# Kernel tuning notes

Hardware: AMD Instinct MI355X
Metric: run time of the kernel (lower is better)

## Reference

```python
import jax, jax.numpy as jnp
import numpy as np

ITERATIONS = 20


def setup_inputs() -> dict:
    key = jax.random.key(0)
    x = jax.random.normal(key, (64, 8, 256, 256), dtype=jnp.float32)
    return {"x": x}


def reference(x):
    # Sinkhorn operator in log space: 20 alternating row/col log-softmax,
    # then exponentiate to obtain a (soft) doubly-stochastic matrix.
    def body(i, x):
        x = jax.nn.log_softmax(x, axis=-2)  # normalize columns
        x = jax.nn.log_softmax(x, axis=-1)  # normalize rows
        return x

    x = jax.lax.fori_loop(0, ITERATIONS, body, x)
    return jnp.exp(x)
```

## Files before the change

kernel.cpp:

```cpp
#include <hip/hip_runtime.h>

#define MAT_N 256
#define TPB   512
#define ITERS 20

typedef _Float16 half2v __attribute__((ext_vector_type(2)));

template<int CTRL>
__device__ __forceinline__ float dpp_add(float x) {
    int s = __builtin_amdgcn_update_dpp(0, __builtin_bit_cast(int, x), CTRL, 0xF, 0xF, true);
    return x + __builtin_bit_cast(float, s);
}
__device__ __forceinline__ float allreduce16(float x) {
    x = dpp_add<0x121>(x);
    x = dpp_add<0x122>(x);
    x = dpp_add<0x124>(x);
    x = dpp_add<0x128>(x);
    return x;
}

__device__ __forceinline__ half2v pkrtz(float lo, float hi) {
    return __builtin_bit_cast(half2v, __builtin_amdgcn_cvt_pkrtz(lo, hi));
}

#if __has_builtin(__builtin_amdgcn_fdot2)
__device__ __forceinline__ float dot2(half2v a, half2v b, float c) {
    return __builtin_amdgcn_fdot2(a, b, c, false);
}
#else
__device__ __forceinline__ float dot2(half2v a, half2v b, float c) {
    return c + (float)a.x * (float)b.x + (float)a.y * (float)b.y;
}
#endif

__global__ __launch_bounds__(TPB)
__attribute__((amdgpu_waves_per_eu(4, 4)))
void sinkhorn_kernel(const float* __restrict__ x, float* __restrict__ out)
{
    const int t    = threadIdx.x;
    const int tC   = t & 15;
    const int tR   = t >> 4;
    const int row0 = tR << 3;
    const int col0 = tC << 4;

    const size_t moff = (size_t)blockIdx.x * (MAT_N * MAT_N);
    const float* __restrict__ xm = x + moff;
    float* __restrict__       om = out + moff;

    __shared__ half2v part[32][132];
    __shared__ float  gvec[MAT_N];

    half2v E[8][8];
#pragma unroll
    for (int l = 0; l < 8; ++l) {
        const float* rp = xm + (row0 + l) * MAT_N + col0;
        float4 a = ((const float4*)rp)[0];
        float4 b = ((const float4*)rp)[1];
        float4 c = ((const float4*)rp)[2];
        float4 d = ((const float4*)rp)[3];
        E[l][0] = (half2v){(_Float16)__expf(a.x), (_Float16)__expf(a.y)};
        E[l][1] = (half2v){(_Float16)__expf(a.z), (_Float16)__expf(a.w)};
        E[l][2] = (half2v){(_Float16)__expf(b.x), (_Float16)__expf(b.y)};
        E[l][3] = (half2v){(_Float16)__expf(b.z), (_Float16)__expf(b.w)};
        E[l][4] = (half2v){(_Float16)__expf(c.x), (_Float16)__expf(c.y)};
        E[l][5] = (half2v){(_Float16)__expf(c.z), (_Float16)__expf(c.w)};
        E[l][6] = (half2v){(_Float16)__expf(d.x), (_Float16)__expf(d.y)};
        E[l][7] = (half2v){(_Float16)__expf(d.z), (_Float16)__expf(d.w)};
    }

    float  f[8];
    half2v f2[8];
#pragma unroll
    for (int l = 0; l < 8; ++l) {
        f[l]  = 1.0f;
        f2[l] = (half2v){(_Float16)1.0f, (_Float16)1.0f};
    }
    half2v g2[8];

    for (int it = 0; it < ITERS; ++it) {
        half2v p2[8];
#pragma unroll
        for (int k = 0; k < 8; ++k) p2[k] = E[0][k] * f2[0];
#pragma unroll
        for (int l = 1; l < 8; ++l)
#pragma unroll
            for (int k = 0; k < 8; ++k) p2[k] += E[l][k] * f2[l];

        {
            half2v* wp = &part[tR][tC << 3];
            float4 w0 = make_float4(__builtin_bit_cast(float, p2[0]),
                                    __builtin_bit_cast(float, p2[1]),
                                    __builtin_bit_cast(float, p2[2]),
                                    __builtin_bit_cast(float, p2[3]));
            float4 w1 = make_float4(__builtin_bit_cast(float, p2[4]),
                                    __builtin_bit_cast(float, p2[5]),
                                    __builtin_bit_cast(float, p2[6]),
                                    __builtin_bit_cast(float, p2[7]));
            ((float4*)wp)[0] = w0;
            ((float4*)wp)[1] = w1;
        }
        __syncthreads();

        if (t < 128) {
            float slo = 0.0f, shi = 0.0f;
#pragma unroll
            for (int r = 0; r < 32; ++r) {
                half2v v = part[r][t];
                slo += (float)v.x;
                shi += (float)v.y;
            }
            float2 gw;
            gw.x = __builtin_amdgcn_rcpf(slo);
            gw.y = __builtin_amdgcn_rcpf(shi);
            *(float2*)&gvec[t << 1] = gw;
        }
        __syncthreads();

        {
            const float* gp = &gvec[col0];
            float4 a = ((const float4*)gp)[0];
            float4 b = ((const float4*)gp)[1];
            float4 c = ((const float4*)gp)[2];
            float4 d = ((const float4*)gp)[3];
            g2[0] = pkrtz(a.x, a.y);
            g2[1] = pkrtz(a.z, a.w);
            g2[2] = pkrtz(b.x, b.y);
            g2[3] = pkrtz(b.z, b.w);
            g2[4] = pkrtz(c.x, c.y);
            g2[5] = pkrtz(c.z, c.w);
            g2[6] = pkrtz(d.x, d.y);
            g2[7] = pkrtz(d.z, d.w);
        }

#pragma unroll
        for (int l = 0; l < 8; ++l) {
            float s = dot2(E[l][0], g2[0], 0.0f);
#pragma unroll
            for (int k = 1; k < 8; ++k) s = dot2(E[l][k], g2[k], s);
            s = allreduce16(s);
            f[l] = __builtin_amdgcn_rcpf(s);
            _Float16 h = (_Float16)f[l];
            f2[l] = (half2v){h, h};
        }
    }

    float g[16];
    {
        const float* gp = &gvec[col0];
        float4 a = ((const float4*)gp)[0];
        float4 b = ((const float4*)gp)[1];
        float4 c = ((const float4*)gp)[2];
        float4 d = ((const float4*)gp)[3];
        g[0]=a.x;  g[1]=a.y;  g[2]=a.z;  g[3]=a.w;
        g[4]=b.x;  g[5]=b.y;  g[6]=b.z;  g[7]=b.w;
        g[8]=c.x;  g[9]=c.y;  g[10]=c.z; g[11]=c.w;
        g[12]=d.x; g[13]=d.y; g[14]=d.z; g[15]=d.w;
    }
#pragma unroll
    for (int l = 0; l < 8; ++l) {
        float fr = f[l];
        float* rp = om + (row0 + l) * MAT_N + col0;
        float o[16];
#pragma unroll
        for (int k = 0; k < 8; ++k) {
            o[2*k]   = (float)E[l][k].x * fr * g[2*k];
            o[2*k+1] = (float)E[l][k].y * fr * g[2*k+1];
        }
        ((float4*)rp)[0] = make_float4(o[0],  o[1],  o[2],  o[3]);
        ((float4*)rp)[1] = make_float4(o[4],  o[5],  o[6],  o[7]);
        ((float4*)rp)[2] = make_float4(o[8],  o[9],  o[10], o[11]);
        ((float4*)rp)[3] = make_float4(o[12], o[13], o[14], o[15]);
    }
}

extern "C" void kernel_launch(void* const* d_in, const int* in_sizes, int n_in,
                              void* d_out, int out_size, void* d_ws, size_t ws_size,
                              hipStream_t stream) {
    const float* x = (const float*)d_in[0];
    float* out = (float*)d_out;
    const int nmat = in_sizes[0] / (MAT_N * MAT_N);
    sinkhorn_kernel<<<nmat, TPB, 0, stream>>>(x, out);
}
```

Baseline: 270.8 us.

## Parallelize column-sum reduction across all threads with DPP and padded LDS

The column reduction is spread over all 512 threads instead of only 128. Each thread sums 8 of the 32 partial rows, and the four partial sums are combined with DPP row shifts. The partial buffer is padded to a new stride with per-group offsets to avoid LDS bank conflicts. The reciprocal g is also stored pre-packed as fp16 pairs, so the broadcast read becomes two 16-byte loads with no conversion. This shortens the serial reduction phase between barriers, at the cost of more complex indexing and extra LDS.

```diff
diff --git a/kernel.cpp b/kernel.cpp
--- a/kernel.cpp
+++ b/kernel.cpp
@@ -3,6 +3,7 @@
 #define MAT_N 256
 #define TPB   512
 #define ITERS 20
+#define PSTRIDE 164
 
 typedef _Float16 half2v __attribute__((ext_vector_type(2)));
 
@@ -18,6 +19,11 @@
     x = dpp_add<0x128>(x);
     return x;
 }
+__device__ __forceinline__ float reduce4spaced(float x) {
+    x = dpp_add<0x124>(x);
+    x = dpp_add<0x128>(x);
+    return x;
+}
 
 __device__ __forceinline__ half2v pkrtz(float lo, float hi) {
     return __builtin_bit_cast(half2v, __builtin_amdgcn_cvt_pkrtz(lo, hi));
@@ -32,6 +38,7 @@
     return c + (float)a.x * (float)b.x + (float)a.y * (float)b.y;
 }
 #endif
+
 
 __global__ __launch_bounds__(TPB)
 __attribute__((amdgpu_waves_per_eu(4, 4)))
@@ -42,12 +49,19 @@
     const int tR   = t >> 4;
     const int row0 = tR << 3;
     const int col0 = tC << 4;
+    const int pbase = (tC << 3) + ((tC >> 2) << 2);
+
+    const int rl   = t & 15;
+    const int rw   = ((t >> 4) << 2) + (rl & 3);
+    const int rrow = rl >> 2;
+    const int rpos = rw + ((rw >> 5) << 2);
 
     const size_t moff = (size_t)blockIdx.x * (MAT_N * MAT_N);
     const float* __restrict__ xm = x + moff;
     float* __restrict__       om = out + moff;
 
-    __shared__ half2v part[32][132];
+    __shared__ half2v part[32 * PSTRIDE];
+    __shared__ half2v g2p[140];
     __shared__ float  gvec[MAT_N];
 
     half2v E[8][8];
@@ -77,6 +91,9 @@
     }
     half2v g2[8];
 
+    half2v* const wp = &part[tR * PSTRIDE + pbase];
+    const half2v* const rdp = &part[rrow * PSTRIDE + rpos];
+
     for (int it = 0; it < ITERS; ++it) {
         half2v p2[8];
 #pragma unroll
@@ -87,7 +104,6 @@
             for (int k = 0; k < 8; ++k) p2[k] += E[l][k] * f2[l];
 
         {
-            half2v* wp = &part[tR][tC << 3];
             float4 w0 = make_float4(__builtin_bit_cast(float, p2[0]),
                                     __builtin_bit_cast(float, p2[1]),
                                     __builtin_bit_cast(float, p2[2]),
@@ -97,39 +113,40 @@
                                     __builtin_bit_cast(float, p2[6]),
                                     __builtin_bit_cast(float, p2[7]));
             ((float4*)wp)[0] = w0;
-            ((float4*)wp)[1] = w1;
+            ((float4*)(wp + 4))[0] = w1;
         }
         __syncthreads();
 
-        if (t < 128) {
+        {
             float slo = 0.0f, shi = 0.0f;
 #pragma unroll
-            for (int r = 0; r < 32; ++r) {
-                half2v v = part[r][t];
+            for (int i = 0; i < 8; ++i) {
+                half2v v = rdp[(i << 2) * PSTRIDE];
                 slo += (float)v.x;
                 shi += (float)v.y;
             }
-            float2 gw;
-            gw.x = __builtin_amdgcn_rcpf(slo);
-            gw.y = __builtin_amdgcn_rcpf(shi);
-            *(float2*)&gvec[t << 1] = gw;
+            slo = reduce4spaced(slo);
+            shi = reduce4spaced(shi);
+            if (rl < 4) {
+                float glo = __builtin_amdgcn_rcpf(slo);
+                float ghi = __builtin_amdgcn_rcpf(shi);
+                *(float2*)&gvec[rw << 1] = make_float2(glo, ghi);
+                g2p[rpos] = pkrtz(glo, ghi);
+            }
         }
         __syncthreads();
 
         {
-            const float* gp = &gvec[col0];
-            float4 a = ((const float4*)gp)[0];
-            float4 b = ((const float4*)gp)[1];
-            float4 c = ((const float4*)gp)[2];
-            float4 d = ((const float4*)gp)[3];
-            g2[0] = pkrtz(a.x, a.y);
-            g2[1] = pkrtz(a.z, a.w);
-            g2[2] = pkrtz(b.x, b.y);
-            g2[3] = pkrtz(b.z, b.w);
-            g2[4] = pkrtz(c.x, c.y);
-            g2[5] = pkrtz(c.z, c.w);
-            g2[6] = pkrtz(d.x, d.y);
-            g2[7] = pkrtz(d.z, d.w);
+            const float4 ga = ((const float4*)&g2p[pbase])[0];
+            const float4 gb = ((const float4*)&g2p[pbase + 4])[0];
+            g2[0] = __builtin_bit_cast(half2v, ga.x);
+            g2[1] = __builtin_bit_cast(half2v, ga.y);
+            g2[2] = __builtin_bit_cast(half2v, ga.z);
+            g2[3] = __builtin_bit_cast(half2v, ga.w);
+            g2[4] = __builtin_bit_cast(half2v, gb.x);
+            g2[5] = __builtin_bit_cast(half2v, gb.y);
+            g2[6] = __builtin_bit_cast(half2v, gb.z);
+            g2[7] = __builtin_bit_cast(half2v, gb.w);
         }
 
 #pragma unroll
```

After: 259.4 us. 1.04x faster.

## Keep transposed copy of E in registers for DPP-based column reductions

Applied to the files above, without the earlier changes.

Builds a transposed fp16 copy of the exp matrix in registers through a shared-memory staging pass. Column sums then use the same dot2-plus-DPP reduction pattern as row sums. This replaces the shared-memory partial-sum write and the serial 32-row reduction done by 128 threads. Each iteration now exchanges only the f and g scaling vectors through small padded LDS buffers. The cost is doubled register storage for E (high pressure at 4 waves/EU) and a one-time transpose with extra barriers.

```diff
diff --git a/kernel.cpp b/kernel.cpp
--- a/kernel.cpp
+++ b/kernel.cpp
@@ -3,6 +3,7 @@
 #define MAT_N 256
 #define TPB   512
 #define ITERS 20
+#define TSTRIDE 72
 
 typedef _Float16 half2v __attribute__((ext_vector_type(2)));
 
@@ -18,11 +19,9 @@
     x = dpp_add<0x128>(x);
     return x;
 }
-
 __device__ __forceinline__ half2v pkrtz(float lo, float hi) {
     return __builtin_bit_cast(half2v, __builtin_amdgcn_cvt_pkrtz(lo, hi));
 }
-
 #if __has_builtin(__builtin_amdgcn_fdot2)
 __device__ __forceinline__ float dot2(half2v a, half2v b, float c) {
     return __builtin_amdgcn_fdot2(a, b, c, false);
@@ -38,17 +37,23 @@
 void sinkhorn_kernel(const float* __restrict__ x, float* __restrict__ out)
 {
     const int t    = threadIdx.x;
-    const int tC   = t & 15;
-    const int tR   = t >> 4;
-    const int row0 = tR << 3;
-    const int col0 = tC << 4;
+    const int g16  = t >> 4;
+    const int rl   = t & 15;
+    const int row0 = g16 << 3;
+    const int col0 = rl << 4;
+
+    const int pb_fg  = (rl << 3) + ((rl >> 2) << 2);
+    const int wWrite = (g16 << 2) + rl;
+    const int pWrite = wWrite + ((wWrite >> 5) << 2);
 
     const size_t moff = (size_t)blockIdx.x * (MAT_N * MAT_N);
     const float* __restrict__ xm = x + moff;
     float* __restrict__       om = out + moff;
 
-    __shared__ half2v part[32][132];
-    __shared__ float  gvec[MAT_N];
+    __shared__ __align__(16) _Float16 stage[256 * TSTRIDE];
+    __shared__ __align__(16) half2v   fbuf[140];
+    __shared__ __align__(16) half2v   gbuf[140];
+    __shared__ float2 gf[128];
 
     half2v E[8][8];
 #pragma unroll
@@ -68,103 +73,122 @@
         E[l][7] = (half2v){(_Float16)__expf(d.z), (_Float16)__expf(d.w)};
     }
 
-    float  f[8];
-    half2v f2[8];
+    if (t < 140) fbuf[t] = (half2v){(_Float16)1.0f, (_Float16)1.0f};
+
+    half2v ET[8][8];
+#pragma unroll
+    for (int q = 0; q < 4; ++q) {
+        if ((rl >> 2) == q) {
+            const int coff = (rl & 3) << 4;
+#pragma unroll
+            for (int l = 0; l < 8; ++l) {
+                const int idx = (row0 + l) * TSTRIDE + coff;
+                *(float4*)&stage[idx] = make_float4(
+                    __builtin_bit_cast(float, E[l][0]), __builtin_bit_cast(float, E[l][1]),
+                    __builtin_bit_cast(float, E[l][2]), __builtin_bit_cast(float, E[l][3]));
+                *(float4*)&stage[idx + 8] = make_float4(
+                    __builtin_bit_cast(float, E[l][4]), __builtin_bit_cast(float, E[l][5]),
+                    __builtin_bit_cast(float, E[l][6]), __builtin_bit_cast(float, E[l][7]));
+            }
+        }
+        __syncthreads();
+        if ((g16 >> 3) == q) {
+            const int coff = (g16 & 7) << 3;
+#pragma unroll
+            for (int j = 0; j < 8; ++j) {
+                float4 ra = *(const float4*)&stage[((rl << 4) + (j << 1)) * TSTRIDE + coff];
+                float4 rb = *(const float4*)&stage[((rl << 4) + (j << 1) + 1) * TSTRIDE + coff];
+                half2v a0 = __builtin_bit_cast(half2v, ra.x), b0 = __builtin_bit_cast(half2v, rb.x);
+                half2v a1 = __builtin_bit_cast(half2v, ra.y), b1 = __builtin_bit_cast(half2v, rb.y);
+                half2v a2 = __builtin_bit_cast(half2v, ra.z), b2 = __builtin_bit_cast(half2v, rb.z);
+                half2v a3 = __builtin_bit_cast(half2v, ra.w), b3 = __builtin_bit_cast(half2v, rb.w);
+                ET[0][j] = (half2v){a0.x, b0.x};  ET[1][j] = (half2v){a0.y, b0.y};
+                ET[2][j] = (half2v){a1.x, b1.x};  ET[3][j] = (half2v){a1.y, b1.y};
+                ET[4][j] = (half2v){a2.x, b2.x};  ET[5][j] = (half2v){a2.y, b2.y};
+                ET[6][j] = (half2v){a3.x, b3.x};  ET[7][j] = (half2v){a3.y, b3.y};
+            }
+        }
+        __syncthreads();
+    }
+
+    float fv[8];
+
+    for (int it = 0; it < ITERS; ++it) {
+        float4 fa = *(const float4*)&fbuf[pb_fg];
+        float4 fb = *(const float4*)&fbuf[pb_fg + 4];
+        half2v fp0 = __builtin_bit_cast(half2v, fa.x), fp1 = __builtin_bit_cast(half2v, fa.y);
+        half2v fp2 = __builtin_bit_cast(half2v, fa.z), fp3 = __builtin_bit_cast(half2v, fa.w);
+        half2v fp4 = __builtin_bit_cast(half2v, fb.x), fp5 = __builtin_bit_cast(half2v, fb.y);
+        half2v fp6 = __builtin_bit_cast(half2v, fb.z), fp7 = __builtin_bit_cast(half2v, fb.w);
+
+        float gv[8];
+#pragma unroll
+        for (int c = 0; c < 8; ++c) {
+            float s = dot2(ET[c][0], fp0, 0.0f);
+            s = dot2(ET[c][1], fp1, s);
+            s = dot2(ET[c][2], fp2, s);
+            s = dot2(ET[c][3], fp3, s);
+            s = dot2(ET[c][4], fp4, s);
+            s = dot2(ET[c][5], fp5, s);
+            s = dot2(ET[c][6], fp6, s);
+            s = dot2(ET[c][7], fp7, s);
+            s = allreduce16(s);
+            gv[c] = __builtin_amdgcn_rcpf(s);
+        }
+        {
+            float glo = rl == 1 ? gv[2] : rl == 2 ? gv[4] : rl == 3 ? gv[6] : gv[0];
+            float ghi = rl == 1 ? gv[3] : rl == 2 ? gv[5] : rl == 3 ? gv[7] : gv[1];
+            if (rl < 4) {
+                gbuf[pWrite] = pkrtz(glo, ghi);
+                if (it == ITERS - 1) gf[wWrite] = make_float2(glo, ghi);
+            }
+        }
+        __syncthreads();
+
+        float4 ga = *(const float4*)&gbuf[pb_fg];
+        float4 gb = *(const float4*)&gbuf[pb_fg + 4];
+        half2v g0 = __builtin_bit_cast(half2v, ga.x), g1 = __builtin_bit_cast(half2v, ga.y);
+        half2v g2 = __builtin_bit_cast(half2v, ga.z), g3 = __builtin_bit_cast(half2v, ga.w);
+        half2v g4 = __builtin_bit_cast(half2v, gb.x), g5 = __builtin_bit_cast(half2v, gb.y);
+        half2v g6 = __builtin_bit_cast(half2v, gb.z), g7 = __builtin_bit_cast(half2v, gb.w);
+
+#pragma unroll
+        for (int l = 0; l < 8; ++l) {
+            float s = dot2(E[l][0], g0, 0.0f);
+            s = dot2(E[l][1], g1, s);
+            s = dot2(E[l][2], g2, s);
+            s = dot2(E[l][3], g3, s);
+            s = dot2(E[l][4], g4, s);
+            s = dot2(E[l][5], g5, s);
+            s = dot2(E[l][6], g6, s);
+            s = dot2(E[l][7], g7, s);
+            s = allreduce16(s);
+            fv[l] = __builtin_amdgcn_rcpf(s);
+        }
+        {
+            float flo = rl == 1 ? fv[2] : rl == 2 ? fv[4] : rl == 3 ? fv[6] : fv[0];
+            float fhi = rl == 1 ? fv[3] : rl == 2 ? fv[5] : rl == 3 ? fv[7] : fv[1];
+            if (rl < 4) fbuf[pWrite] = pkrtz(flo, fhi);
+        }
+        __syncthreads();
+    }
+
+    float Gc[16];
+#pragma unroll
+    for (int i = 0; i < 8; ++i) {
+        float2 gg = gf[(rl << 3) + i];
+        Gc[2 * i]     = gg.x;
+        Gc[2 * i + 1] = gg.y;
+    }
 #pragma unroll
     for (int l = 0; l < 8; ++l) {
-        f[l]  = 1.0f;
-        f2[l] = (half2v){(_Float16)1.0f, (_Float16)1.0f};
-    }
-    half2v g2[8];
-
-    for (int it = 0; it < ITERS; ++it) {
-        half2v p2[8];
-#pragma unroll
-        for (int k = 0; k < 8; ++k) p2[k] = E[0][k] * f2[0];
-#pragma unroll
-        for (int l = 1; l < 8; ++l)
-#pragma unroll
-            for (int k = 0; k < 8; ++k) p2[k] += E[l][k] * f2[l];
-
-        {
-            half2v* wp = &part[tR][tC << 3];
-            float4 w0 = make_float4(__builtin_bit_cast(float, p2[0]),
-                                    __builtin_bit_cast(float, p2[1]),
-                                    __builtin_bit_cast(float, p2[2]),
-                                    __builtin_bit_cast(float, p2[3]));
-            float4 w1 = make_float4(__builtin_bit_cast(float, p2[4]),
-                                    __builtin_bit_cast(float, p2[5]),
-                                    __builtin_bit_cast(float, p2[6]),
-                                    __builtin_bit_cast(float, p2[7]));
-            ((float4*)wp)[0] = w0;
-            ((float4*)wp)[1] = w1;
-        }
-        __syncthreads();
-
-        if (t < 128) {
-            float slo = 0.0f, shi = 0.0f;
-#pragma unroll
-            for (int r = 0; r < 32; ++r) {
-                half2v v = part[r][t];
-                slo += (float)v.x;
-                shi += (float)v.y;
-            }
-            float2 gw;
-            gw.x = __builtin_amdgcn_rcpf(slo);
-            gw.y = __builtin_amdgcn_rcpf(shi);
-            *(float2*)&gvec[t << 1] = gw;
-        }
-        __syncthreads();
-
-        {
-            const float* gp = &gvec[col0];
-            float4 a = ((const float4*)gp)[0];
-            float4 b = ((const float4*)gp)[1];
-            float4 c = ((const float4*)gp)[2];
-            float4 d = ((const float4*)gp)[3];
-            g2[0] = pkrtz(a.x, a.y);
-            g2[1] = pkrtz(a.z, a.w);
-            g2[2] = pkrtz(b.x, b.y);
-            g2[3] = pkrtz(b.z, b.w);
-            g2[4] = pkrtz(c.x, c.y);
-            g2[5] = pkrtz(c.z, c.w);
-            g2[6] = pkrtz(d.x, d.y);
-            g2[7] = pkrtz(d.z, d.w);
-        }
-
-#pragma unroll
-        for (int l = 0; l < 8; ++l) {
-            float s = dot2(E[l][0], g2[0], 0.0f);
-#pragma unroll
-            for (int k = 1; k < 8; ++k) s = dot2(E[l][k], g2[k], s);
-            s = allreduce16(s);
-            f[l] = __builtin_amdgcn_rcpf(s);
-            _Float16 h = (_Float16)f[l];
-            f2[l] = (half2v){h, h};
-        }
-    }
-
-    float g[16];
-    {
-        const float* gp = &gvec[col0];
-        float4 a = ((const float4*)gp)[0];
-        float4 b = ((const float4*)gp)[1];
-        float4 c = ((const float4*)gp)[2];
-        float4 d = ((const float4*)gp)[3];
-        g[0]=a.x;  g[1]=a.y;  g[2]=a.z;  g[3]=a.w;
-        g[4]=b.x;  g[5]=b.y;  g[6]=b.z;  g[7]=b.w;
-        g[8]=c.x;  g[9]=c.y;  g[10]=c.z; g[11]=c.w;
-        g[12]=d.x; g[13]=d.y; g[14]=d.z; g[15]=d.w;
-    }
-#pragma unroll
-    for (int l = 0; l < 8; ++l) {
-        float fr = f[l];
+        float fr = fv[l];
         float* rp = om + (row0 + l) * MAT_N + col0;
         float o[16];
 #pragma unroll
         for (int k = 0; k < 8; ++k) {
-            o[2*k]   = (float)E[l][k].x * fr * g[2*k];
-            o[2*k+1] = (float)E[l][k].y * fr * g[2*k+1];
+            o[2 * k]     = (float)E[l][k].x * fr * Gc[2 * k];
+            o[2 * k + 1] = (float)E[l][k].y * fr * Gc[2 * k + 1];
         }
         ((float4*)rp)[0] = make_float4(o[0],  o[1],  o[2],  o[3]);
         ((float4*)rp)[1] = make_float4(o[4],  o[5],  o[6],  o[7]);
```

New measurement: 330.1 us. +21.9%, slower.
